# Performance work log

Hardware: AMD Instinct MI355X
Metric: run time of the kernel (lower is better)

The kernel has to match this reference:

```python
import jax, jax.numpy as jnp
import numpy as np

H = 8
DH = 64
MAX_REL = 32
SCALE = DH ** -0.5


def setup_inputs() -> dict:
    key = jax.random.key(0)
    ks = jax.random.split(key, 10)
    B, T, D = 2, 2048, 512
    s = 1.0 / np.sqrt(D)
    return {
        "hidden_states": jax.random.normal(ks[0], (B, T, D), jnp.float32),
        "Wq": jax.random.normal(ks[1], (D, H * DH), jnp.float32) * s,
        "bq": jax.random.normal(ks[2], (H * DH,), jnp.float32) * 0.02,
        "Wk": jax.random.normal(ks[3], (D, H * DH), jnp.float32) * s,
        "bk": jax.random.normal(ks[4], (H * DH,), jnp.float32) * 0.02,
        "Wv": jax.random.normal(ks[5], (D, H * DH), jnp.float32) * s,
        "bv": jax.random.normal(ks[6], (H * DH,), jnp.float32) * 0.02,
        "Wo": jax.random.normal(ks[7], (H * DH, D), jnp.float32) * s,
        "bo": jax.random.normal(ks[8], (D,), jnp.float32) * 0.02,
        "rel_bias": jax.random.normal(ks[9], (H, 2 * MAX_REL + 1), jnp.float32) * 0.02,
    }


def _rel_pos_bias(rel_bias, Tq, Tk):
    # (H, Tq, Tk) additive bias from clamped relative distances
    rel = jnp.arange(Tq)[:, None] - jnp.arange(Tk)[None, :]
    idx = jnp.clip(rel, -MAX_REL, MAX_REL) + MAX_REL
    return rel_bias[:, idx]


def reference(hidden_states, Wq, bq, Wk, bk, Wv, bv, Wo, bo, rel_bias):
    B, T, D = hidden_states.shape
    # projections (enn.Linear == dense linear map in forward math)
    Q = (hidden_states @ Wq + bq).reshape(B, T, H, DH)
    K = (hidden_states @ Wk + bk).reshape(B, T, H, DH)
    V = (hidden_states @ Wv + bv).reshape(B, T, H, DH)
    attn = jnp.einsum("bthd,bkhd->bhtk", Q, K) * SCALE
    attn = attn + _rel_pos_bias(rel_bias, T, T)[None]
    attn = jax.nn.softmax(attn, axis=-1)
    out = jnp.einsum("bhtk,bkhd->bthd", attn, V).reshape(B, T, H * DH)
    return out @ Wo + bo
```

## Files before the change

### kernel.cpp

```cpp
#include <hip/hip_runtime.h>
#include <stdint.h>
#include <math.h>

#define H 8
#define DH 64
#define T 2048
#define D 512
#define B 2
#define BH 16
#define MAXREL 32
#define NREL (2*MAXREL+1)
#define C1 0.18033688f
#define NW (D*D)
#define NSPLIT 4
#define NKIT (T/NSPLIT/64)

typedef _Float16 half_t;
typedef half_t half8 __attribute__((ext_vector_type(8)));
typedef half_t half4 __attribute__((ext_vector_type(4)));
typedef float f32x4 __attribute__((ext_vector_type(4)));
typedef int int4v __attribute__((ext_vector_type(4)));

typedef __attribute__((address_space(3))) unsigned int lds_uint;
typedef const __attribute__((address_space(1))) unsigned int glb_uint;

__device__ __forceinline__ void gl_lds16(const void* g, void* l) {
    __builtin_amdgcn_global_load_lds((glb_uint*)g, (lds_uint*)l, 16, 0, 0);
}
__device__ __forceinline__ f32x4 zero4() { f32x4 z = {0.f,0.f,0.f,0.f}; return z; }
__device__ __forceinline__ int pkrtz(float a, float b) {
    return __builtin_bit_cast(int, __builtin_amdgcn_cvt_pkrtz(a, b));
}

__global__ __launch_bounds__(256) void prep(
    const float* __restrict__ X,
    const float* __restrict__ Wq, const float* __restrict__ Wk,
    const float* __restrict__ Wv, const float* __restrict__ Wo,
    half_t* __restrict__ Xh, half_t* __restrict__ Wts)
{
    __shared__ half_t Ld[64 * 72];
    const int bid = blockIdx.x;
    const int tid = threadIdx.x;
    if (bid < 1024) {
        const int i = (bid * 256 + tid) * 8;
        const float4 a = *(const float4*)(X + i);
        const float4 b = *(const float4*)(X + i + 4);
        half8 o;
        o[0]=(half_t)a.x; o[1]=(half_t)a.y; o[2]=(half_t)a.z; o[3]=(half_t)a.w;
        o[4]=(half_t)b.x; o[5]=(half_t)b.y; o[6]=(half_t)b.z; o[7]=(half_t)b.w;
        *(half8*)(Xh + i) = o;
    } else {
        const int id = bid - 1024;
        const int z = id >> 6;
        const int tile = id & 63;
        const float* __restrict__ W = (z==0)?Wq:(z==1)?Wk:(z==2)?Wv:Wo;
        half_t* __restrict__ out = Wts + (size_t)z * NW;
        const int k0 = (tile >> 3) * 64;
        const int n0 = (tile & 7) * 64;
        const int r = tid >> 2, c16 = (tid & 3) * 16;
        const float* src = W + (size_t)(k0 + r) * D + n0 + c16;
        #pragma unroll
        for (int j = 0; j < 16; ++j) Ld[r * 72 + c16 + j] = (half_t)src[j];
        __syncthreads();
        half_t tmp[16];
        #pragma unroll
        for (int j = 0; j < 16; ++j) tmp[j] = Ld[(c16 + j) * 72 + r];
        half8* dst = (half8*)(out + (size_t)(n0 + r) * D + k0 + c16);
        dst[0] = *(half8*)&tmp[0];
        dst[1] = *(half8*)&tmp[8];
    }
}

__global__ __launch_bounds__(256) void gemm_qkv(
    const half_t* __restrict__ Xh, const half_t* __restrict__ Wts,
    const float* __restrict__ bq, const float* __restrict__ bk,
    const float* __restrict__ bv,
    half_t* __restrict__ Qh, half_t* __restrict__ Kh, half_t* __restrict__ Vth)
{
    __shared__ half_t As[2][64 * 64];
    __shared__ half_t Bs[2][128 * 64];
    const int tid = threadIdx.x, w = tid >> 6, lane = tid & 63;
    const int l15 = lane & 15, quad = lane >> 4;
    const int m0 = blockIdx.x * 64, n0 = blockIdx.y * 128, z = blockIdx.z;
    const half_t* __restrict__ Wt = Wts + (size_t)z * NW;
    const float* __restrict__ bias = (z==0)?bq:(z==1)?bk:bv;

    auto stage = [&](int buf, int k0) {
        #pragma unroll
        for (int s = 0; s < 2; ++s) {
            const int cid = (w * 2 + s) * 64 + lane;
            const int r = cid >> 3, c = (cid & 7) ^ (r & 7);
            gl_lds16(Xh + (size_t)(m0 + r) * D + k0 + c * 8,
                     &As[buf][(w * 2 + s) * 512]);
        }
        #pragma unroll
        for (int s = 0; s < 4; ++s) {
            const int cid = (w * 4 + s) * 64 + lane;
            const int r = cid >> 3, c = (cid & 7) ^ (r & 7);
            gl_lds16(Wt + (size_t)(n0 + r) * D + k0 + c * 8,
                     &Bs[buf][(w * 4 + s) * 512]);
        }
    };

    f32x4 acc[4][2];
    #pragma unroll
    for (int ms = 0; ms < 4; ++ms) { acc[ms][0] = zero4(); acc[ms][1] = zero4(); }

    stage(0, 0);
    __syncthreads();
    for (int it = 0; it < 8; ++it) {
        const int cur = it & 1;
        if (it < 7) stage(cur ^ 1, (it + 1) * 64);
        const int swiz = l15 & 7;
        #pragma unroll
        for (int ks = 0; ks < 2; ++ks) {
            const int c = (ks * 4 + quad) ^ swiz;
            half8 bf[2];
            #pragma unroll
            for (int nt = 0; nt < 2; ++nt)
                bf[nt] = *(const half8*)&Bs[cur][(w * 32 + nt * 16 + l15) * 64 + c * 8];
            #pragma unroll
            for (int ms = 0; ms < 4; ++ms) {
                const half8 af = *(const half8*)&As[cur][(ms * 16 + l15) * 64 + c * 8];
                acc[ms][0] = __builtin_amdgcn_mfma_f32_16x16x32_f16(af, bf[0], acc[ms][0], 0, 0, 0);
                acc[ms][1] = __builtin_amdgcn_mfma_f32_16x16x32_f16(af, bf[1], acc[ms][1], 0, 0, 0);
            }
        }
        __syncthreads();
    }

    float bvv[2];
    #pragma unroll
    for (int nt = 0; nt < 2; ++nt) bvv[nt] = bias[n0 + w * 32 + nt * 16 + l15];

    if (z == 2) {
        #pragma unroll
        for (int ms = 0; ms < 4; ++ms) {
            const int mbase = m0 + ms * 16 + quad * 4;
            const int bb = mbase >> 11, t0 = mbase & 2047;
            #pragma unroll
            for (int nt = 0; nt < 2; ++nt) {
                const int n = n0 + w * 32 + nt * 16 + l15;
                const int hh = n >> 6, d = n & 63;
                half4 pk;
                #pragma unroll
                for (int r = 0; r < 4; ++r) pk[r] = (half_t)(acc[ms][nt][r] + bvv[nt]);
                *(half4*)(Vth + (((size_t)bb * H + hh) * DH + d) * T + t0) = pk;
            }
        }
    } else {
        half_t* __restrict__ dst = (z == 0) ? Qh : Kh;
        #pragma unroll
        for (int ms = 0; ms < 4; ++ms)
            #pragma unroll
            for (int nt = 0; nt < 2; ++nt)
                #pragma unroll
                for (int r = 0; r < 4; ++r) {
                    const int mrow = m0 + ms * 16 + quad * 4 + r;
                    const int n = n0 + w * 32 + nt * 16 + l15;
                    const int bb = mrow >> 11, t = mrow & 2047, hh = n >> 6, d = n & 63;
                    dst[(((size_t)bb * H + hh) * T + t) * DH + d] = (half_t)(acc[ms][nt][r] + bvv[nt]);
                }
    }
}

__global__ __launch_bounds__(256, 4) void attn_fwd(
    const half_t* __restrict__ Qh, const half_t* __restrict__ Kh,
    const half_t* __restrict__ Vth, const float* __restrict__ relb,
    half_t* __restrict__ On01, half_t* __restrict__ On23,
    half_t* __restrict__ lsum)
{
    __shared__ half_t Kt[2][4096];
    __shared__ half_t Vt[2][4096];
    __shared__ float rb2[NREL];

    const int tid = threadIdx.x, w = tid >> 6, lane = tid & 63;
    const int l15 = lane & 15, quad = lane >> 4;
    const int qw = blockIdx.x * 128 + w * 32;
    const int bh = blockIdx.y;
    const int split = blockIdx.z;
    const int kb0 = split * (T / NSPLIT);
    const int h = bh & 7;

    if (tid < NREL) rb2[tid] = relb[h * NREL + tid] * 1.44269504f;

    half8 qf[2][2];
    const half_t* Qbase = Qh + ((size_t)bh * T + qw) * DH;
    #pragma unroll
    for (int g = 0; g < 2; ++g)
        #pragma unroll
        for (int ks = 0; ks < 2; ++ks)
            qf[g][ks] = *(const half8*)(Qbase + (g * 16 + l15) * DH + ks * 32 + quad * 8);

    f32x4 of[2][4];
    #pragma unroll
    for (int g = 0; g < 2; ++g)
        #pragma unroll
        for (int nt = 0; nt < 4; ++nt) of[g][nt] = zero4();
    float lp[2] = {0.f, 0.f};

    auto stage = [&](int buf, int kb) {
        #pragma unroll
        for (int s = 0; s < 2; ++s) {
            const int cid = (w * 2 + s) * 64 + lane;
            const int r = cid >> 3, cg = (cid & 7) ^ (r & 7);
            gl_lds16(Kh + ((size_t)bh * T + kb + r) * DH + cg * 8,
                     &Kt[buf][(w * 2 + s) * 512]);
            gl_lds16(Vth + ((size_t)bh * DH + r) * T + kb + cg * 8,
                     &Vt[buf][(w * 2 + s) * 512]);
        }
    };

    stage(0, kb0);
    __syncthreads();

    const int swiz = l15 & 7;

    for (int it = 0; it < NKIT; ++it) {
        const int cur = it & 1;
        if (it + 1 < NKIT) stage(cur ^ 1, kb0 + (it + 1) * 64);
        const int kb = kb0 + it * 64;

        f32x4 st[2][4];
        #pragma unroll
        for (int g = 0; g < 2; ++g)
            #pragma unroll
            for (int nt = 0; nt < 4; ++nt) st[g][nt] = zero4();
        #pragma unroll
        for (int ks = 0; ks < 2; ++ks) {
            const int c = (ks * 4 + quad) ^ swiz;
            #pragma unroll
            for (int nt = 0; nt < 4; ++nt) {
                const half8 kf = *(const half8*)&Kt[cur][(nt * 16 + l15) * 64 + c * 8];
                st[0][nt] = __builtin_amdgcn_mfma_f32_16x16x32_f16(kf, qf[0][ks], st[0][nt], 0, 0, 0);
                st[1][nt] = __builtin_amdgcn_mfma_f32_16x16x32_f16(kf, qf[1][ks], st[1][nt], 0, 0, 0);
            }
        }

        int pd[2][4][2];
        const bool uni_hi = (qw - (kb + 63)) >= MAXREL;
        const bool uni_lo = ((qw + 31) - kb) <= -MAXREL;
        if (uni_hi || uni_lo) {
            const float bu = uni_hi ? rb2[NREL - 1] : rb2[0];
            #pragma unroll
            for (int g = 0; g < 2; ++g)
                #pragma unroll
                for (int nt = 0; nt < 4; ++nt) {
                    float p[4];
                    #pragma unroll
                    for (int r = 0; r < 4; ++r) p[r] = exp2f(fmaf(st[g][nt][r], C1, bu));
                    lp[g] += (p[0] + p[1]) + (p[2] + p[3]);
                    pd[g][nt][0] = pkrtz(p[0], p[1]);
                    pd[g][nt][1] = pkrtz(p[2], p[3]);
                }
        } else {
            #pragma unroll
            for (int g = 0; g < 2; ++g) {
                const int qg = qw + g * 16 + l15;
                #pragma unroll
                for (int nt = 0; nt < 4; ++nt) {
                    float p[4];
                    #pragma unroll
                    for (int r = 0; r < 4; ++r) {
                        const int key = kb + nt * 16 + quad * 4 + r;
                        int rel = qg - key;
                        rel = rel < -MAXREL ? -MAXREL : (rel > MAXREL ? MAXREL : rel);
                        p[r] = exp2f(fmaf(st[g][nt][r], C1, rb2[rel + MAXREL]));
                    }
                    lp[g] += (p[0] + p[1]) + (p[2] + p[3]);
                    pd[g][nt][0] = pkrtz(p[0], p[1]);
                    pd[g][nt][1] = pkrtz(p[2], p[3]);
                }
            }
        }

        #pragma unroll
        for (int ks = 0; ks < 2; ++ks) {
            half8 pf[2];
            #pragma unroll
            for (int g = 0; g < 2; ++g) {
                int4v bd;
                #pragma unroll
                for (int d = 0; d < 4; ++d) {
                    const int src = ((quad & 1) * 2 + (d >> 1)) * 16 + l15;
                    const int va = __shfl(pd[g][2 * ks][d & 1], src);
                    const int vb = __shfl(pd[g][2 * ks + 1][d & 1], src);
                    bd[d] = (quad >> 1) ? vb : va;
                }
                pf[g] = __builtin_bit_cast(half8, bd);
            }
            const int c = (ks * 4 + quad) ^ swiz;
            #pragma unroll
            for (int nt = 0; nt < 4; ++nt) {
                const half8 vf = *(const half8*)&Vt[cur][(nt * 16 + l15) * 64 + c * 8];
                of[0][nt] = __builtin_amdgcn_mfma_f32_16x16x32_f16(vf, pf[0], of[0][nt], 0, 0, 0);
                of[1][nt] = __builtin_amdgcn_mfma_f32_16x16x32_f16(vf, pf[1], of[1][nt], 0, 0, 0);
            }
        }
        __syncthreads();
    }

    half_t* Obuf = (split < 2) ? On01 : On23;
    const int sl = split & 1;
    #pragma unroll
    for (int g = 0; g < 2; ++g) {
        const size_t qrow = ((size_t)(sl * BH + bh)) * T + qw + g * 16 + l15;
        half_t* obase = Obuf + qrow * DH;
        #pragma unroll
        for (int nt = 0; nt < 4; ++nt) {
            half4 pk;
            #pragma unroll
            for (int r = 0; r < 4; ++r) pk[r] = (half_t)(of[g][nt][r] * 0.015625f);
            *(half4*)(obase + nt * 16 + quad * 4) = pk;
        }
        float v = lp[g];
        v += __shfl_xor(v, 16);
        v += __shfl_xor(v, 32);
        if (quad == 0)
            lsum[((size_t)(split * BH + bh)) * T + qw + g * 16 + l15] = (half_t)(v * 0.015625f);
    }
}

__global__ __launch_bounds__(256) void combine(
    const half_t* __restrict__ On01, const half_t* __restrict__ On23,
    const half_t* __restrict__ lsum, half_t* __restrict__ AOh)
{
    const int i = blockIdx.x * 256 + threadIdx.x;
    const int r = i >> 6;
    const int c = (i & 63) * 8;
    const int b = r >> 11, t = r & 2047, hh = c >> 6, d = c & 63;
    const int bh = b * H + hh;
    float acc[8] = {};
    float l = 0.f;
    #pragma unroll
    for (int s = 0; s < NSPLIT; ++s) {
        const half_t* Obuf = (s < 2) ? On01 : On23;
        const size_t off = ((size_t)((s & 1) * BH + bh) * T + t) * DH + d;
        const half8 x = *(const half8*)(Obuf + off);
        #pragma unroll
        for (int j = 0; j < 8; ++j) acc[j] += (float)x[j];
        l += (float)lsum[(size_t)(s * BH + bh) * T + t];
    }
    const float inv = 1.0f / l;
    half8 o;
    #pragma unroll
    for (int j = 0; j < 8; ++j) o[j] = (half_t)(acc[j] * inv);
    *(half8*)(AOh + (size_t)r * D + c) = o;
}

__global__ __launch_bounds__(256) void gemm_out(
    const half_t* __restrict__ AOh, const half_t* __restrict__ Wot,
    const float* __restrict__ bo, float* __restrict__ out)
{
    __shared__ half_t As[2][32 * 64];
    __shared__ half_t Bs[2][128 * 64];
    const int tid = threadIdx.x, w = tid >> 6, lane = tid & 63;
    const int l15 = lane & 15, quad = lane >> 4;
    const int m0 = blockIdx.x * 32, n0 = blockIdx.y * 128;

    auto stage = [&](int buf, int k0) {
        {
            const int cid = w * 64 + lane;
            const int r = cid >> 3, c = (cid & 7) ^ (r & 7);
            gl_lds16(AOh + (size_t)(m0 + r) * D + k0 + c * 8,
                     &As[buf][w * 512]);
        }
        #pragma unroll
        for (int s = 0; s < 4; ++s) {
            const int cid = (w * 4 + s) * 64 + lane;
            const int r = cid >> 3, c = (cid & 7) ^ (r & 7);
            gl_lds16(Wot + (size_t)(n0 + r) * D + k0 + c * 8,
                     &Bs[buf][(w * 4 + s) * 512]);
        }
    };

    f32x4 acc[2][2];
    #pragma unroll
    for (int ms = 0; ms < 2; ++ms) { acc[ms][0] = zero4(); acc[ms][1] = zero4(); }

    stage(0, 0);
    __syncthreads();
    for (int it = 0; it < 8; ++it) {
        const int cur = it & 1;
        if (it < 7) stage(cur ^ 1, (it + 1) * 64);
        const int swiz = l15 & 7;
        #pragma unroll
        for (int ks = 0; ks < 2; ++ks) {
            const int c = (ks * 4 + quad) ^ swiz;
            half8 bf[2];
            #pragma unroll
            for (int nt = 0; nt < 2; ++nt)
                bf[nt] = *(const half8*)&Bs[cur][(w * 32 + nt * 16 + l15) * 64 + c * 8];
            #pragma unroll
            for (int ms = 0; ms < 2; ++ms) {
                const half8 af = *(const half8*)&As[cur][(ms * 16 + l15) * 64 + c * 8];
                acc[ms][0] = __builtin_amdgcn_mfma_f32_16x16x32_f16(af, bf[0], acc[ms][0], 0, 0, 0);
                acc[ms][1] = __builtin_amdgcn_mfma_f32_16x16x32_f16(af, bf[1], acc[ms][1], 0, 0, 0);
            }
        }
        __syncthreads();
    }

    float bvv[2];
    #pragma unroll
    for (int nt = 0; nt < 2; ++nt) bvv[nt] = bo[n0 + w * 32 + nt * 16 + l15];
    #pragma unroll
    for (int ms = 0; ms < 2; ++ms)
        #pragma unroll
        for (int nt = 0; nt < 2; ++nt)
            #pragma unroll
            for (int r = 0; r < 4; ++r) {
                const int mrow = m0 + ms * 16 + quad * 4 + r;
                const int n = n0 + w * 32 + nt * 16 + l15;
                out[(size_t)mrow * D + n] = acc[ms][nt][r] + bvv[nt];
            }
}

extern "C" void kernel_launch(void* const* d_in, const int* in_sizes, int n_in,
                              void* d_out, int out_size, void* d_ws, size_t ws_size,
                              hipStream_t stream)
{
    const float* hs   = (const float*)d_in[0];
    const float* Wq   = (const float*)d_in[1];
    const float* bq   = (const float*)d_in[2];
    const float* Wk   = (const float*)d_in[3];
    const float* bk   = (const float*)d_in[4];
    const float* Wv   = (const float*)d_in[5];
    const float* bv   = (const float*)d_in[6];
    const float* Wo   = (const float*)d_in[7];
    const float* bo   = (const float*)d_in[8];
    const float* relb = (const float*)d_in[9];

    const size_t NX = (size_t)B * T * D;
    half_t* wsh = (half_t*)d_ws;
    half_t* Xh  = wsh;
    half_t* Wts = Xh + NX;
    half_t* Qh  = Wts + 4 * (size_t)NW;
    half_t* Kh  = Qh + NX;
    half_t* Vth = Kh + NX;
    half_t* On23 = Vth + NX;
    half_t* Ls  = On23 + 2 * NX;
    half_t* On01 = (half_t*)d_out;
    half_t* AOh = Xh;

    prep    <<<dim3(1280), 256, 0, stream>>>(hs, Wq, Wk, Wv, Wo, Xh, Wts);
    gemm_qkv<<<dim3(64, 4, 3), 256, 0, stream>>>(Xh, Wts, bq, bk, bv, Qh, Kh, Vth);
    attn_fwd<<<dim3(16, BH, NSPLIT), 256, 0, stream>>>(Qh, Kh, Vth, relb, On01, On23, Ls);
    combine <<<dim3(1024), 256, 0, stream>>>(On01, On23, Ls, AOh);
    gemm_out<<<dim3(128, 4), 256, 0, stream>>>(AOh, Wts + 3 * (size_t)NW, bo, (float*)d_out);
}
```

Measured before the change: 153.5 us.

## Load K/V fragments directly from global memory and drop P shuffles via 16x16x16 MFMA

Removes the double-buffered LDS staging of K and V tiles and its per-iteration barrier, so each wave reads its K and V MFMA fragments straight from global memory (relying on L1/L2 reuse across waves). The PV product switches from 16x16x32 to 16x16x16 MFMA so the packed probability registers already match the B-operand layout, removing the cross-lane shuffles. Occupancy hint drops from 4 to 3 blocks. The cost is more global or cache traffic with no prefetch overlap, and twice as many, smaller MFMA instructions for PV.

```diff
diff --git a/kernel.cpp b/kernel.cpp
--- a/kernel.cpp
+++ b/kernel.cpp
@@ -19,7 +19,7 @@
 typedef half_t half8 __attribute__((ext_vector_type(8)));
 typedef half_t half4 __attribute__((ext_vector_type(4)));
 typedef float f32x4 __attribute__((ext_vector_type(4)));
-typedef int int4v __attribute__((ext_vector_type(4)));
+typedef int int2v __attribute__((ext_vector_type(2)));
 
 typedef __attribute__((address_space(3))) unsigned int lds_uint;
 typedef const __attribute__((address_space(1))) unsigned int glb_uint;
@@ -164,14 +164,12 @@
     }
 }
 
-__global__ __launch_bounds__(256, 4) void attn_fwd(
+__global__ __launch_bounds__(256, 3) void attn_fwd(
     const half_t* __restrict__ Qh, const half_t* __restrict__ Kh,
     const half_t* __restrict__ Vth, const float* __restrict__ relb,
     half_t* __restrict__ On01, half_t* __restrict__ On23,
     half_t* __restrict__ lsum)
 {
-    __shared__ half_t Kt[2][4096];
-    __shared__ half_t Vt[2][4096];
     __shared__ float rb2[NREL];
 
     const int tid = threadIdx.x, w = tid >> 6, lane = tid & 63;
@@ -183,6 +181,7 @@
     const int h = bh & 7;
 
     if (tid < NREL) rb2[tid] = relb[h * NREL + tid] * 1.44269504f;
+    __syncthreads();
 
     half8 qf[2][2];
     const half_t* Qbase = Qh + ((size_t)bh * T + qw) * DH;
@@ -192,33 +191,17 @@
         for (int ks = 0; ks < 2; ++ks)
             qf[g][ks] = *(const half8*)(Qbase + (g * 16 + l15) * DH + ks * 32 + quad * 8);
 
+    const half_t* Kp = Kh + (size_t)bh * T * DH;
+    const half_t* Vp = Vth + (size_t)bh * DH * T;
+
     f32x4 of[2][4];
     #pragma unroll
     for (int g = 0; g < 2; ++g)
         #pragma unroll
-        for (int nt = 0; nt < 4; ++nt) of[g][nt] = zero4();
+        for (int mt = 0; mt < 4; ++mt) of[g][mt] = zero4();
     float lp[2] = {0.f, 0.f};
 
-    auto stage = [&](int buf, int kb) {
-        #pragma unroll
-        for (int s = 0; s < 2; ++s) {
-            const int cid = (w * 2 + s) * 64 + lane;
-            const int r = cid >> 3, cg = (cid & 7) ^ (r & 7);
-            gl_lds16(Kh + ((size_t)bh * T + kb + r) * DH + cg * 8,
-                     &Kt[buf][(w * 2 + s) * 512]);
-            gl_lds16(Vth + ((size_t)bh * DH + r) * T + kb + cg * 8,
-                     &Vt[buf][(w * 2 + s) * 512]);
-        }
-    };
-
-    stage(0, kb0);
-    __syncthreads();
-
-    const int swiz = l15 & 7;
-
     for (int it = 0; it < NKIT; ++it) {
-        const int cur = it & 1;
-        if (it + 1 < NKIT) stage(cur ^ 1, kb0 + (it + 1) * 64);
         const int kb = kb0 + it * 64;
 
         f32x4 st[2][4];
@@ -227,17 +210,16 @@
             #pragma unroll
             for (int nt = 0; nt < 4; ++nt) st[g][nt] = zero4();
         #pragma unroll
-        for (int ks = 0; ks < 2; ++ks) {
-            const int c = (ks * 4 + quad) ^ swiz;
+        for (int ks = 0; ks < 2; ++ks)
             #pragma unroll
             for (int nt = 0; nt < 4; ++nt) {
-                const half8 kf = *(const half8*)&Kt[cur][(nt * 16 + l15) * 64 + c * 8];
+                const half8 kf = *(const half8*)(Kp + (size_t)(kb + nt * 16 + l15) * DH
+                                                 + ks * 32 + quad * 8);
                 st[0][nt] = __builtin_amdgcn_mfma_f32_16x16x32_f16(kf, qf[0][ks], st[0][nt], 0, 0, 0);
                 st[1][nt] = __builtin_amdgcn_mfma_f32_16x16x32_f16(kf, qf[1][ks], st[1][nt], 0, 0, 0);
             }
-        }
-
-        int pd[2][4][2];
+
+        half4 pf[2][4];
         const bool uni_hi = (qw - (kb + 63)) >= MAXREL;
         const bool uni_lo = ((qw + 31) - kb) <= -MAXREL;
         if (uni_hi || uni_lo) {
@@ -250,8 +232,8 @@
                     #pragma unroll
                     for (int r = 0; r < 4; ++r) p[r] = exp2f(fmaf(st[g][nt][r], C1, bu));
                     lp[g] += (p[0] + p[1]) + (p[2] + p[3]);
-                    pd[g][nt][0] = pkrtz(p[0], p[1]);
-                    pd[g][nt][1] = pkrtz(p[2], p[3]);
+                    int2v pk; pk[0] = pkrtz(p[0], p[1]); pk[1] = pkrtz(p[2], p[3]);
+                    pf[g][nt] = __builtin_bit_cast(half4, pk);
                 }
         } else {
             #pragma unroll
@@ -268,36 +250,22 @@
                         p[r] = exp2f(fmaf(st[g][nt][r], C1, rb2[rel + MAXREL]));
                     }
                     lp[g] += (p[0] + p[1]) + (p[2] + p[3]);
-                    pd[g][nt][0] = pkrtz(p[0], p[1]);
-                    pd[g][nt][1] = pkrtz(p[2], p[3]);
+                    int2v pk; pk[0] = pkrtz(p[0], p[1]); pk[1] = pkrtz(p[2], p[3]);
+                    pf[g][nt] = __builtin_bit_cast(half4, pk);
                 }
             }
         }
 
         #pragma unroll
-        for (int ks = 0; ks < 2; ++ks) {
-            half8 pf[2];
-            #pragma unroll
-            for (int g = 0; g < 2; ++g) {
-                int4v bd;
-                #pragma unroll
-                for (int d = 0; d < 4; ++d) {
-                    const int src = ((quad & 1) * 2 + (d >> 1)) * 16 + l15;
-                    const int va = __shfl(pd[g][2 * ks][d & 1], src);
-                    const int vb = __shfl(pd[g][2 * ks + 1][d & 1], src);
-                    bd[d] = (quad >> 1) ? vb : va;
-                }
-                pf[g] = __builtin_bit_cast(half8, bd);
-            }
-            const int c = (ks * 4 + quad) ^ swiz;
-            #pragma unroll
-            for (int nt = 0; nt < 4; ++nt) {
-                const half8 vf = *(const half8*)&Vt[cur][(nt * 16 + l15) * 64 + c * 8];
-                of[0][nt] = __builtin_amdgcn_mfma_f32_16x16x32_f16(vf, pf[0], of[0][nt], 0, 0, 0);
-                of[1][nt] = __builtin_amdgcn_mfma_f32_16x16x32_f16(vf, pf[1], of[1][nt], 0, 0, 0);
-            }
-        }
-        __syncthreads();
+        for (int nt = 0; nt < 4; ++nt) {
+            #pragma unroll
+            for (int mt = 0; mt < 4; ++mt) {
+                const half4 vf = *(const half4*)(Vp + (size_t)(mt * 16 + l15) * T
+                                                 + kb + nt * 16 + quad * 4);
+                of[0][mt] = __builtin_amdgcn_mfma_f32_16x16x16f16(vf, pf[0][nt], of[0][mt], 0, 0, 0);
+                of[1][mt] = __builtin_amdgcn_mfma_f32_16x16x16f16(vf, pf[1][nt], of[1][mt], 0, 0, 0);
+            }
+        }
     }
 
     half_t* Obuf = (split < 2) ? On01 : On23;
@@ -307,11 +275,11 @@
         const size_t qrow = ((size_t)(sl * BH + bh)) * T + qw + g * 16 + l15;
         half_t* obase = Obuf + qrow * DH;
         #pragma unroll
-        for (int nt = 0; nt < 4; ++nt) {
+        for (int mt = 0; mt < 4; ++mt) {
             half4 pk;
             #pragma unroll
-            for (int r = 0; r < 4; ++r) pk[r] = (half_t)(of[g][nt][r] * 0.015625f);
-            *(half4*)(obase + nt * 16 + quad * 4) = pk;
+            for (int r = 0; r < 4; ++r) pk[r] = (half_t)(of[g][mt][r] * 0.015625f);
+            *(half4*)(obase + mt * 16 + quad * 4) = pk;
         }
         float v = lp[g];
         v += __shfl_xor(v, 16);
```

New measurement: 200.3 us. +30.5%, slower.
